# Kernel optimization log

Measured on AMD Instinct MI355X. Metric: run time of the kernel, lower is better.

## Reference

```python
import jax, jax.numpy as jnp
import numpy as np

USER_SIZE = 100000
ITEM_SIZE = 50000
LATENT = 256
BATCH = 8192
ALPHA = 0.8
TAU = 3.0
SHRINK_NORM = 1.0


def setup_inputs() -> dict:
    key = jax.random.key(0)
    k1, k2, k3, k4 = jax.random.split(key, 4)
    # xavier-uniform style init like the torch code
    bu = np.sqrt(6.0 / (USER_SIZE + LATENT)).astype(np.float32)
    bi = np.sqrt(6.0 / (ITEM_SIZE + LATENT)).astype(np.float32)
    user_embed = jax.random.uniform(k1, (USER_SIZE, LATENT), jnp.float32, -bu, bu)
    item_embed = jax.random.uniform(k2, (ITEM_SIZE, LATENT), jnp.float32, -bi, bi)
    u = jax.random.randint(k3, (BATCH,), 0, USER_SIZE)
    p = jax.random.randint(k4, (BATCH,), 0, ITEM_SIZE)
    return {"user_embed": user_embed, "item_embed": item_embed, "u": u, "p": p}


def _spec_smooth(x):
    # x: [B, d] row-normalized embeddings
    # x - alpha * softmax(x x^T * tau, axis=1) @ x, then shrink-norm rescale
    attn = jax.nn.softmax(jnp.einsum('bd,cd->bc', x, x) * TAU, axis=1)  # [B, B]
    y = x - ALPHA * (attn @ x)
    # shrink_norm != 0 branch (static config)
    norm = jnp.linalg.norm(y, axis=1, keepdims=True)
    return y * (norm * SHRINK_NORM)


def reference(user_embed, item_embed, u, p):
    fu = user_embed[u]
    fp = item_embed[p]
    fu = fu / jnp.linalg.norm(fu, axis=1, keepdims=True)
    fp = fp / jnp.linalg.norm(fp, axis=1, keepdims=True)
    fu = _spec_smooth(fu)
    fp = _spec_smooth(fp)
    out = jax.nn.sigmoid(jnp.sum(fu * fp, axis=1))  # [B]
    return -jnp.sum(jnp.log(out)) / BATCH
```

## Files before the change

kernel.cpp:

```cpp
#include <hip/hip_runtime.h>
#include <hip/hip_bf16.h>

#define B_ROWS 8192
#define D_DIM  256
#define QB     64
#define KB     64
#define NT     (B_ROWS / KB)
#define NT2    (NT / 2)
#define ALPHA  0.8f
#define TAU_LOG2E 4.328085122666890f

typedef __attribute__((ext_vector_type(8))) short bf16x8;
typedef __attribute__((ext_vector_type(4))) float f32x4;
typedef __attribute__((ext_vector_type(4))) unsigned short ushort4v;

__device__ inline unsigned short f2bf(float f) {
    unsigned int u = __builtin_bit_cast(unsigned int, f);
    u += 0x7FFF + ((u >> 16) & 1);
    return (unsigned short)(u >> 16);
}

__device__ inline void gl_lds16(const void* g, void* l) {
    __builtin_amdgcn_global_load_lds(
        (const __attribute__((address_space(1))) unsigned int*)g,
        (__attribute__((address_space(3))) unsigned int*)l, 16, 0, 0);
}

__device__ inline void barrier_lgkm() {
    asm volatile("s_waitcnt lgkmcnt(0)" ::: "memory");
    __builtin_amdgcn_s_barrier();
    asm volatile("" ::: "memory");
}
__device__ inline void barrier_all() {
    asm volatile("s_waitcnt vmcnt(0) lgkmcnt(0)" ::: "memory");
    __builtin_amdgcn_s_barrier();
    asm volatile("" ::: "memory");
}

__global__ __launch_bounds__(256) void k_gather_norm(
    const float* __restrict__ ue, const float* __restrict__ ie,
    const int* __restrict__ u, const int* __restrict__ p,
    float* __restrict__ Xf, unsigned short* __restrict__ Xh,
    float* __restrict__ out)
{
    const int b = blockIdx.x * 4 + (threadIdx.x >> 6);
    const int lane = threadIdx.x & 63;
    if (b == 0 && lane == 0) out[0] = 0.0f;
    const int m = b >> 13;
    const int r = b & 8191;
    const float* src = (m == 0) ? (ue + (size_t)u[r] * D_DIM)
                                : (ie + (size_t)p[r] * D_DIM);
    float4 v = ((const float4*)src)[lane];
    float ss = v.x*v.x + v.y*v.y + v.z*v.z + v.w*v.w;
    #pragma unroll
    for (int mask = 32; mask; mask >>= 1) ss += __shfl_xor(ss, mask);
    const float inv = 1.0f / sqrtf(ss);
    v.x *= inv; v.y *= inv; v.z *= inv; v.w *= inv;
    const size_t off = (size_t)(m * B_ROWS + r) * D_DIM + lane * 4;
    *(float4*)(Xf + off) = v;
    ushort4v h = { f2bf(v.x), f2bf(v.y), f2bf(v.z), f2bf(v.w) };
    *(ushort4v*)(Xh + off) = h;
}

__global__ __launch_bounds__(256) void k_transpose(
    const unsigned short* __restrict__ Xh, unsigned short* __restrict__ Xht)
{
    __shared__ unsigned short tile[64 * 84];
    const int bid = blockIdx.x;
    const int m = bid >> 9;
    const int t = bid & 511;
    const int rt = t >> 2, ct = t & 3;
    const int r0 = rt * 64, c0 = ct * 64;
    const int tid = threadIdx.x;
    const unsigned short* src = Xh + (size_t)m * B_ROWS * D_DIM;
    unsigned short* dst = Xht + (size_t)m * D_DIM * B_ROWS;
    #pragma unroll
    for (int ph = 0; ph < 2; ++ph) {
        const int row = ph * 32 + (tid >> 3);
        const int ch = tid & 7;
        const unsigned short* s = src + (size_t)(r0 + row) * D_DIM + c0 + ch * 8;
        ushort4v a = *(const ushort4v*)s;
        ushort4v b = *(const ushort4v*)(s + 4);
        *(ushort4v*)(&tile[row * 84 + ch * 8]) = a;
        *(ushort4v*)(&tile[row * 84 + ch * 8 + 4]) = b;
    }
    __syncthreads();
    #pragma unroll
    for (int ph = 0; ph < 2; ++ph) {
        const int d = ph * 32 + (tid >> 3);
        const int kc = tid & 7;
        ushort4v lo = { tile[(kc*8+0)*84 + d], tile[(kc*8+1)*84 + d],
                        tile[(kc*8+2)*84 + d], tile[(kc*8+3)*84 + d] };
        ushort4v hi = { tile[(kc*8+4)*84 + d], tile[(kc*8+5)*84 + d],
                        tile[(kc*8+6)*84 + d], tile[(kc*8+7)*84 + d] };
        unsigned short* o = dst + (size_t)(c0 + d) * B_ROWS + r0 + kc * 8;
        *(ushort4v*)o = lo;
        *(ushort4v*)(o + 4) = hi;
    }
}

__global__ __launch_bounds__(512, 2) void k_flash_part(
    const unsigned short* __restrict__ Xh,
    const unsigned short* __restrict__ Xht,
    float* __restrict__ Opart,
    float* __restrict__ lsum_part)
{
    __shared__ unsigned char Kls[64 * 512];
    __shared__ unsigned char Vtls[256 * 128];
    __shared__ unsigned char Pls[64 * 128];
    __shared__ float lsum_sh[4][QB];

    const int tid = threadIdx.x;
    const int lane = tid & 63;
    const int w = tid >> 6;
    const int wm = w >> 2;
    const int wn = w & 3;
    const int m  = blockIdx.x >> 8;
    const int qb = (blockIdx.x >> 1) & 127;
    const int h  = blockIdx.x & 1;
    const int q0 = qb * QB;
    const int kvbase = h * (B_ROWS / 2);

    const unsigned short* Xm  = Xh  + (size_t)m * B_ROWS * D_DIM;
    const unsigned short* Xtm = Xht + (size_t)m * D_DIM * B_ROWS;

    bf16x8 qf[2][8];
    #pragma unroll
    for (int mi = 0; mi < 2; ++mi) {
        const unsigned short* qbp = Xm + (size_t)(q0 + wm*32 + mi*16 + (lane & 15)) * D_DIM
                                       + (lane >> 4) * 8;
        #pragma unroll
        for (int kk = 0; kk < 8; ++kk)
            qf[mi][kk] = *(const bf16x8*)(qbp + kk * 32);
    }

    const int kchunk0 = w * 4;
    const int krow_l  = (lane >> 5);
    const int kcol16  = lane & 31;
    const int vd_l    = (lane >> 3);
    const int vkc16   = lane & 7;

    #pragma unroll
    for (int it = 0; it < 4; ++it) {
        const int chunk = kchunk0 + it;
        const int krow = chunk * 2 + krow_l;
        const int kdch = kcol16 ^ (krow & 7);
        gl_lds16(Xm + (size_t)(kvbase + krow) * D_DIM + kdch * 8, &Kls[chunk * 1024]);
        const int vd = chunk * 8 + vd_l;
        const int vkc = vkc16 ^ (vd & 7);
        gl_lds16(Xtm + (size_t)vd * B_ROWS + kvbase + vkc * 8, &Vtls[chunk * 1024]);
    }

    f32x4 o[2][4];
    #pragma unroll
    for (int mi = 0; mi < 2; ++mi)
        #pragma unroll
        for (int nf = 0; nf < 4; ++nf) o[mi][nf] = (f32x4){0.f, 0.f, 0.f, 0.f};
    float lsum[2][4] = {{0.f,0.f,0.f,0.f},{0.f,0.f,0.f,0.f}};

    for (int kt = 0; kt < NT2; ++kt) {
        barrier_all();

        f32x4 s0 = {0.f,0.f,0.f,0.f}, s1 = {0.f,0.f,0.f,0.f};
        {
            const int brow = wn * 16 + (lane & 15);
            const unsigned char* kbase = &Kls[brow * 512];
            const int bswz = (brow & 7) << 4;
            __builtin_amdgcn_s_setprio(1);
            #pragma unroll
            for (int kk = 0; kk < 8; ++kk) {
                const int kb = kk * 64 + ((lane >> 4) * 16);
                bf16x8 bK = *(const bf16x8*)(kbase + (kb ^ bswz));
                s0 = __builtin_amdgcn_mfma_f32_16x16x32_bf16(qf[0][kk], bK, s0, 0, 0, 0);
                s1 = __builtin_amdgcn_mfma_f32_16x16x32_bf16(qf[1][kk], bK, s1, 0, 0, 0);
            }
            __builtin_amdgcn_s_setprio(0);
        }
        #pragma unroll
        for (int i = 0; i < 4; ++i) {
            const float p0 = exp2f(s0[i] * TAU_LOG2E);
            const float p1 = exp2f(s1[i] * TAU_LOG2E);
            lsum[0][i] += p0;
            lsum[1][i] += p1;
            const int pr0 = wm*32 + (lane >> 4) * 4 + i;
            const int pr1 = pr0 + 16;
            const int pc2 = (wn*16 + (lane & 15)) * 2;
            *(unsigned short*)(Pls + pr0*128 + (pc2 ^ ((pr0 & 7) << 4))) = f2bf(p0);
            *(unsigned short*)(Pls + pr1*128 + (pc2 ^ ((pr1 & 7) << 4))) = f2bf(p1);
        }
        barrier_lgkm();

        bf16x8 aP[2][2];
        #pragma unroll
        for (int mi = 0; mi < 2; ++mi)
            #pragma unroll
            for (int ks = 0; ks < 2; ++ks) {
                const int ar = wm*32 + mi*16 + (lane & 15);
                const int akb = ks*64 + ((lane >> 4) * 16);
                aP[mi][ks] = *(const bf16x8*)(Pls + ar*128 + (akb ^ ((ar & 7) << 4)));
            }
        __builtin_amdgcn_s_setprio(1);
        #pragma unroll
        for (int ks = 0; ks < 2; ++ks) {
            #pragma unroll
            for (int nf = 0; nf < 4; ++nf) {
                const int dr = wn*64 + nf*16 + (lane & 15);
                const int kb2 = ks*64 + ((lane >> 4) * 16);
                bf16x8 bV = *(const bf16x8*)(&Vtls[dr*128 + (kb2 ^ ((dr & 7) << 4))]);
                o[0][nf] = __builtin_amdgcn_mfma_f32_16x16x32_bf16(aP[0][ks], bV, o[0][nf], 0, 0, 0);
                o[1][nf] = __builtin_amdgcn_mfma_f32_16x16x32_bf16(aP[1][ks], bV, o[1][nf], 0, 0, 0);
            }
        }
        __builtin_amdgcn_s_setprio(0);
        barrier_lgkm();

        if (kt + 1 < NT2) {
            const int kvn = kvbase + (kt + 1) * KB;
            #pragma unroll
            for (int it = 0; it < 4; ++it) {
                const int chunk = kchunk0 + it;
                const int krow = chunk * 2 + krow_l;
                const int kdch = kcol16 ^ (krow & 7);
                gl_lds16(Xm + (size_t)(kvn + krow) * D_DIM + kdch * 8, &Kls[chunk * 1024]);
                const int vd = chunk * 8 + vd_l;
                const int vkc = vkc16 ^ (vd & 7);
                gl_lds16(Xtm + (size_t)vd * B_ROWS + kvn + vkc * 8, &Vtls[chunk * 1024]);
            }
        }
    }

    #pragma unroll
    for (int mi = 0; mi < 2; ++mi)
        #pragma unroll
        for (int i = 0; i < 4; ++i) {
            float v = lsum[mi][i];
            v += __shfl_xor(v, 1); v += __shfl_xor(v, 2);
            v += __shfl_xor(v, 4); v += __shfl_xor(v, 8);
            if ((lane & 15) == 0)
                lsum_sh[wn][wm*32 + mi*16 + (lane >> 4)*4 + i] = v;
        }
    __syncthreads();
    if (tid < QB)
        lsum_part[(size_t)blockIdx.x * QB + tid] =
            lsum_sh[0][tid] + lsum_sh[1][tid] + lsum_sh[2][tid] + lsum_sh[3][tid];

    float* Ob = Opart + (size_t)blockIdx.x * QB * D_DIM;
    #pragma unroll
    for (int mi = 0; mi < 2; ++mi)
        #pragma unroll
        for (int nf = 0; nf < 4; ++nf)
            #pragma unroll
            for (int i = 0; i < 4; ++i) {
                const int row = wm*32 + mi*16 + (lane >> 4)*4 + i;
                const int col = wn*64 + nf*16 + (lane & 15);
                Ob[row * D_DIM + col] = o[mi][nf][i];
            }
}

__global__ __launch_bounds__(256) void k_combine_loss(
    const float* __restrict__ Xf, const float* __restrict__ Opart,
    const float* __restrict__ lsum_part, float* __restrict__ out)
{
    __shared__ float part[4];
    const int w = threadIdx.x >> 6;
    const int lane = threadIdx.x & 63;
    const int r = blockIdx.x * 4 + w;
    const int qb = r >> 6, ri = r & 63;

    float y[2][4];
    float nrm[2];
    #pragma unroll
    for (int m = 0; m < 2; ++m) {
        const int blk0 = m * 256 + qb * 2;
        const float l = lsum_part[(size_t)blk0 * QB + ri]
                      + lsum_part[(size_t)(blk0 + 1) * QB + ri];
        const float c = ALPHA / l;
        const float4 x  = *(const float4*)(Xf + ((size_t)m * B_ROWS + r) * D_DIM + lane * 4);
        const float4 o0 = *(const float4*)(Opart + ((size_t)blk0 * QB + ri) * D_DIM + lane * 4);
        const float4 o1 = *(const float4*)(Opart + ((size_t)(blk0 + 1) * QB + ri) * D_DIM + lane * 4);
        y[m][0] = x.x - c * (o0.x + o1.x);
        y[m][1] = x.y - c * (o0.y + o1.y);
        y[m][2] = x.z - c * (o0.z + o1.z);
        y[m][3] = x.w - c * (o0.w + o1.w);
        float s = y[m][0]*y[m][0] + y[m][1]*y[m][1] + y[m][2]*y[m][2] + y[m][3]*y[m][3];
        #pragma unroll
        for (int mask = 32; mask; mask >>= 1) s += __shfl_xor(s, mask);
        nrm[m] = s;
    }
    float d = y[0][0]*y[1][0] + y[0][1]*y[1][1] + y[0][2]*y[1][2] + y[0][3]*y[1][3];
    #pragma unroll
    for (int mask = 32; mask; mask >>= 1) d += __shfl_xor(d, mask);
    if (lane == 0) {
        const float z = sqrtf(nrm[0] * nrm[1]) * d;
        part[w] = log1pf(expf(-z));
    }
    __syncthreads();
    if (threadIdx.x == 0)
        atomicAdd(out, (part[0] + part[1] + part[2] + part[3]) * (1.0f / 8192.0f));
}

__global__ __launch_bounds__(512, 2) void k_flash(
    const unsigned short* __restrict__ Xh, const unsigned short* __restrict__ Xht,
    float* __restrict__ Xf)
{
    __shared__ unsigned char Kls[2][64 * 512];
    __shared__ unsigned char Vtls[2][256 * 128];
    __shared__ unsigned char Pls[64 * 128];
    __shared__ float lsum_sh[4][QB];
    __shared__ float nrm_sh[4][QB];

    const int tid = threadIdx.x;
    const int lane = tid & 63;
    const int w = tid >> 6;
    const int wm = w >> 2;
    const int wn = w & 3;
    const int m = blockIdx.x >> 7;
    const int q0 = (blockIdx.x & 127) * QB;

    const unsigned short* Xm  = Xh  + (size_t)m * B_ROWS * D_DIM;
    const unsigned short* Xtm = Xht + (size_t)m * D_DIM * B_ROWS;
    float* Xfm = Xf + (size_t)m * B_ROWS * D_DIM;

    bf16x8 qf[2][8];
    #pragma unroll
    for (int mi = 0; mi < 2; ++mi) {
        const unsigned short* qbp = Xm + (size_t)(q0 + wm*32 + mi*16 + (lane & 15)) * D_DIM
                                       + (lane >> 4) * 8;
        #pragma unroll
        for (int kk = 0; kk < 8; ++kk)
            qf[mi][kk] = *(const bf16x8*)(qbp + kk * 32);
    }

    const int kchunk0 = w * 4;
    const int krow_l  = (lane >> 5);
    const int kcol16  = lane & 31;
    const int vd_l    = (lane >> 3);
    const int vkc16   = lane & 7;

    #pragma unroll
    for (int it = 0; it < 4; ++it) {
        const int chunk = kchunk0 + it;
        const int krow = chunk * 2 + krow_l;
        const int kdch = kcol16 ^ (krow & 7);
        gl_lds16(Xm + (size_t)krow * D_DIM + kdch * 8, &Kls[0][chunk * 1024]);
        const int vd = chunk * 8 + vd_l;
        const int vkc = vkc16 ^ (vd & 7);
        gl_lds16(Xtm + (size_t)vd * B_ROWS + vkc * 8, &Vtls[0][chunk * 1024]);
    }
    barrier_all();

    f32x4 o[2][4];
    #pragma unroll
    for (int mi = 0; mi < 2; ++mi)
        #pragma unroll
        for (int nf = 0; nf < 4; ++nf) o[mi][nf] = (f32x4){0.f, 0.f, 0.f, 0.f};
    float lsum[2][4] = {{0.f,0.f,0.f,0.f},{0.f,0.f,0.f,0.f}};
    int cur = 0;

    for (int kt = 0; kt < NT; ++kt) {
        const int nxt = cur ^ 1;
        if (kt + 1 < NT) {
            const int kvn = (kt + 1) * KB;
            #pragma unroll
            for (int it = 0; it < 4; ++it) {
                const int chunk = kchunk0 + it;
                const int krow = chunk * 2 + krow_l;
                const int kdch = kcol16 ^ (krow & 7);
                gl_lds16(Xm + (size_t)(kvn + krow) * D_DIM + kdch * 8, &Kls[nxt][chunk * 1024]);
                const int vd = chunk * 8 + vd_l;
                const int vkc = vkc16 ^ (vd & 7);
                gl_lds16(Xtm + (size_t)vd * B_ROWS + kvn + vkc * 8, &Vtls[nxt][chunk * 1024]);
            }
        }
        f32x4 s0 = {0.f,0.f,0.f,0.f}, s1 = {0.f,0.f,0.f,0.f};
        {
            const int brow = wn * 16 + (lane & 15);
            const unsigned char* kbase = &Kls[cur][brow * 512];
            const int bswz = (brow & 7) << 4;
            #pragma unroll
            for (int kk = 0; kk < 8; ++kk) {
                const int kb = kk * 64 + ((lane >> 4) * 16);
                bf16x8 bK = *(const bf16x8*)(kbase + (kb ^ bswz));
                s0 = __builtin_amdgcn_mfma_f32_16x16x32_bf16(qf[0][kk], bK, s0, 0, 0, 0);
                s1 = __builtin_amdgcn_mfma_f32_16x16x32_bf16(qf[1][kk], bK, s1, 0, 0, 0);
            }
        }
        #pragma unroll
        for (int i = 0; i < 4; ++i) {
            const float p0 = exp2f(s0[i] * TAU_LOG2E);
            const float p1 = exp2f(s1[i] * TAU_LOG2E);
            lsum[0][i] += p0;
            lsum[1][i] += p1;
            const int pr0 = wm*32 + (lane >> 4) * 4 + i;
            const int pr1 = pr0 + 16;
            const int pc2 = (wn*16 + (lane & 15)) * 2;
            *(unsigned short*)(Pls + pr0*128 + (pc2 ^ ((pr0 & 7) << 4))) = f2bf(p0);
            *(unsigned short*)(Pls + pr1*128 + (pc2 ^ ((pr1 & 7) << 4))) = f2bf(p1);
        }
        barrier_lgkm();
        bf16x8 aP[2][2];
        #pragma unroll
        for (int mi = 0; mi < 2; ++mi)
            #pragma unroll
            for (int ks = 0; ks < 2; ++ks) {
                const int ar = wm*32 + mi*16 + (lane & 15);
                const int akb = ks*64 + ((lane >> 4) * 16);
                aP[mi][ks] = *(const bf16x8*)(Pls + ar*128 + (akb ^ ((ar & 7) << 4)));
            }
        #pragma unroll
        for (int ks = 0; ks < 2; ++ks) {
            #pragma unroll
            for (int nf = 0; nf < 4; ++nf) {
                const int dr = wn*64 + nf*16 + (lane & 15);
                const int kb2 = ks*64 + ((lane >> 4) * 16);
                bf16x8 bV = *(const bf16x8*)(&Vtls[cur][dr*128 + (kb2 ^ ((dr & 7) << 4))]);
                o[0][nf] = __builtin_amdgcn_mfma_f32_16x16x32_bf16(aP[0][ks], bV, o[0][nf], 0, 0, 0);
                o[1][nf] = __builtin_amdgcn_mfma_f32_16x16x32_bf16(aP[1][ks], bV, o[1][nf], 0, 0, 0);
            }
        }
        barrier_all();
        cur = nxt;
    }

    #pragma unroll
    for (int mi = 0; mi < 2; ++mi)
        #pragma unroll
        for (int i = 0; i < 4; ++i) {
            float v = lsum[mi][i];
            v += __shfl_xor(v, 1); v += __shfl_xor(v, 2);
            v += __shfl_xor(v, 4); v += __shfl_xor(v, 8);
            if ((lane & 15) == 0)
                lsum_sh[wn][wm*32 + mi*16 + (lane >> 4)*4 + i] = v;
        }
    __syncthreads();

    float nrm[2][4] = {{0.f,0.f,0.f,0.f},{0.f,0.f,0.f,0.f}};
    #pragma unroll
    for (int mi = 0; mi < 2; ++mi)
        #pragma unroll
        for (int nf = 0; nf < 4; ++nf)
            #pragma unroll
            for (int i = 0; i < 4; ++i) {
                const int row = wm*32 + mi*16 + (lane >> 4)*4 + i;
                const int col = wn*64 + nf*16 + (lane & 15);
                const float x = Xfm[(size_t)(q0 + row) * D_DIM + col];
                const float lt = lsum_sh[0][row] + lsum_sh[1][row]
                               + lsum_sh[2][row] + lsum_sh[3][row];
                const float yv = x - (ALPHA / lt) * o[mi][nf][i];
                o[mi][nf][i] = yv;
                nrm[mi][i] += yv * yv;
            }
    #pragma unroll
    for (int mi = 0; mi < 2; ++mi)
        #pragma unroll
        for (int i = 0; i < 4; ++i) {
            float v = nrm[mi][i];
            v += __shfl_xor(v, 1); v += __shfl_xor(v, 2);
            v += __shfl_xor(v, 4); v += __shfl_xor(v, 8);
            if ((lane & 15) == 0)
                nrm_sh[wn][wm*32 + mi*16 + (lane >> 4)*4 + i] = v;
        }
    __syncthreads();
    #pragma unroll
    for (int mi = 0; mi < 2; ++mi)
        #pragma unroll
        for (int nf = 0; nf < 4; ++nf)
            #pragma unroll
            for (int i = 0; i < 4; ++i) {
                const int row = wm*32 + mi*16 + (lane >> 4)*4 + i;
                const int col = wn*64 + nf*16 + (lane & 15);
                const float scale = sqrtf(nrm_sh[0][row] + nrm_sh[1][row]
                                        + nrm_sh[2][row] + nrm_sh[3][row]);
                Xfm[(size_t)(q0 + row) * D_DIM + col] = o[mi][nf][i] * scale;
            }
}

__global__ __launch_bounds__(256) void k_loss(
    const float* __restrict__ Yu, const float* __restrict__ Yp,
    float* __restrict__ out)
{
    __shared__ float part[4];
    const int w = threadIdx.x >> 6;
    const int lane = threadIdx.x & 63;
    float acc = 0.0f;
    #pragma unroll
    for (int r = 0; r < 8; ++r) {
        const int row = blockIdx.x * 32 + w * 8 + r;
        const float4 a = *(const float4*)(Yu + (size_t)row * D_DIM + lane * 4);
        const float4 b = *(const float4*)(Yp + (size_t)row * D_DIM + lane * 4);
        float dot = a.x*b.x + a.y*b.y + a.z*b.z + a.w*b.w;
        #pragma unroll
        for (int mask = 32; mask; mask >>= 1) dot += __shfl_xor(dot, mask);
        if (lane == 0) acc += log1pf(expf(-dot));
    }
    if (lane == 0) part[w] = acc;
    __syncthreads();
    if (threadIdx.x == 0) {
        const float s = part[0] + part[1] + part[2] + part[3];
        atomicAdd(out, s * (1.0f / 8192.0f));
    }
}

extern "C" void kernel_launch(void* const* d_in, const int* in_sizes, int n_in,
                              void* d_out, int out_size, void* d_ws, size_t ws_size,
                              hipStream_t stream) {
    const float* ue = (const float*)d_in[0];
    const float* ie = (const float*)d_in[1];
    const int*   u  = (const int*)d_in[2];
    const int*   p  = (const int*)d_in[3];
    float* out = (float*)d_out;

    char* ws = (char*)d_ws;
    float* Xf            = (float*)ws;
    unsigned short* Xh   = (unsigned short*)(ws + (16u << 20));
    unsigned short* Xht  = (unsigned short*)(ws + (24u << 20));
    float* Opart         = (float*)(ws + (32u << 20));
    float* lsum_part     = (float*)(ws + (64u << 20));

    const size_t need = (64u << 20) + (128u << 10);

    k_gather_norm<<<4096, 256, 0, stream>>>(ue, ie, u, p, Xf, Xh, out);
    k_transpose <<<1024, 256, 0, stream>>>(Xh, Xht);
    if (ws_size >= need) {
        k_flash_part  <<<512, 512, 0, stream>>>(Xh, Xht, Opart, lsum_part);
        k_combine_loss<<<2048, 256, 0, stream>>>(Xf, Opart, lsum_part, out);
    } else {
        k_flash<<<256, 512, 0, stream>>>(Xh, Xht, Xf);
        k_loss <<<256, 256, 0, stream>>>(Xf, Xf + (size_t)B_ROWS * D_DIM, out);
    }
}
```

Baseline: 454.2 us.

## Double query tile to 128 rows and double-buffer K/V in split flash kernel

Each block of the split-KV flash kernel now processes 128 query rows instead of 64, with each wave holding four 16-row query fragments. This halves the grid and doubles reuse of each K/V tile loaded into LDS. K and V tiles are now double-buffered so the next tile's global-to-LDS load overlaps the current tile's MFMA work. The cost is more LDS and registers per block, and with only 256 blocks on a large-CU device, occupancy and load balance may suffer. The combine kernel's indexing is updated to match the new partial layout, and the setprio hints are dropped.

New measurement: 417.8 us. 1.09x faster.

```diff
diff --git a/kernel.cpp b/kernel.cpp
--- a/kernel.cpp
+++ b/kernel.cpp
@@ -3,10 +3,7 @@
 
 #define B_ROWS 8192
 #define D_DIM  256
-#define QB     64
 #define KB     64
-#define NT     (B_ROWS / KB)
-#define NT2    (NT / 2)
 #define ALPHA  0.8f
 #define TAU_LOG2E 4.328085122666890f
 
@@ -105,29 +102,29 @@
     float* __restrict__ Opart,
     float* __restrict__ lsum_part)
 {
-    __shared__ unsigned char Kls[64 * 512];
-    __shared__ unsigned char Vtls[256 * 128];
-    __shared__ unsigned char Pls[64 * 128];
-    __shared__ float lsum_sh[4][QB];
+    __shared__ unsigned char Kls[2][64 * 512];
+    __shared__ unsigned char Vtls[2][256 * 128];
+    __shared__ unsigned char Pls[128 * 128];
+    __shared__ float lsum_sh[4][128];
 
     const int tid = threadIdx.x;
     const int lane = tid & 63;
     const int w = tid >> 6;
     const int wm = w >> 2;
     const int wn = w & 3;
-    const int m  = blockIdx.x >> 8;
-    const int qb = (blockIdx.x >> 1) & 127;
+    const int m  = blockIdx.x >> 7;
+    const int qb = (blockIdx.x >> 1) & 63;
     const int h  = blockIdx.x & 1;
-    const int q0 = qb * QB;
+    const int q0 = qb * 128;
     const int kvbase = h * (B_ROWS / 2);
 
     const unsigned short* Xm  = Xh  + (size_t)m * B_ROWS * D_DIM;
     const unsigned short* Xtm = Xht + (size_t)m * D_DIM * B_ROWS;
 
-    bf16x8 qf[2][8];
-    #pragma unroll
-    for (int mi = 0; mi < 2; ++mi) {
-        const unsigned short* qbp = Xm + (size_t)(q0 + wm*32 + mi*16 + (lane & 15)) * D_DIM
+    bf16x8 qf[4][8];
+    #pragma unroll
+    for (int mi = 0; mi < 4; ++mi) {
+        const unsigned short* qbp = Xm + (size_t)(q0 + wm*64 + mi*16 + (lane & 15)) * D_DIM
                                        + (lane >> 4) * 8;
         #pragma unroll
         for (int kk = 0; kk < 8; ++kk)
@@ -140,16 +137,221 @@
     const int vd_l    = (lane >> 3);
     const int vkc16   = lane & 7;
 
+    const int brow  = wn * 16 + (lane & 15);
+    const int bswz  = (brow & 7) << 4;
+    const int kqoff = (lane >> 4) * 16;
+
     #pragma unroll
     for (int it = 0; it < 4; ++it) {
         const int chunk = kchunk0 + it;
         const int krow = chunk * 2 + krow_l;
         const int kdch = kcol16 ^ (krow & 7);
-        gl_lds16(Xm + (size_t)(kvbase + krow) * D_DIM + kdch * 8, &Kls[chunk * 1024]);
+        gl_lds16(Xm + (size_t)(kvbase + krow) * D_DIM + kdch * 8, &Kls[0][chunk * 1024]);
         const int vd = chunk * 8 + vd_l;
         const int vkc = vkc16 ^ (vd & 7);
-        gl_lds16(Xtm + (size_t)vd * B_ROWS + kvbase + vkc * 8, &Vtls[chunk * 1024]);
-    }
+        gl_lds16(Xtm + (size_t)vd * B_ROWS + kvbase + vkc * 8, &Vtls[0][chunk * 1024]);
+    }
+    barrier_all();
+
+    f32x4 o[4][4];
+    #pragma unroll
+    for (int mi = 0; mi < 4; ++mi)
+        #pragma unroll
+        for (int nf = 0; nf < 4; ++nf) o[mi][nf] = (f32x4){0.f, 0.f, 0.f, 0.f};
+    float lsum[4][4] = {{0.f,0.f,0.f,0.f},{0.f,0.f,0.f,0.f},
+                        {0.f,0.f,0.f,0.f},{0.f,0.f,0.f,0.f}};
+    int cur = 0;
+
+    for (int kt = 0; kt < 64; ++kt) {
+        const int nxt = cur ^ 1;
+        if (kt + 1 < 64) {
+            const int kvn = kvbase + (kt + 1) * KB;
+            #pragma unroll
+            for (int it = 0; it < 4; ++it) {
+                const int chunk = kchunk0 + it;
+                const int krow = chunk * 2 + krow_l;
+                const int kdch = kcol16 ^ (krow & 7);
+                gl_lds16(Xm + (size_t)(kvn + krow) * D_DIM + kdch * 8,
+                         &Kls[nxt][chunk * 1024]);
+                const int vd = chunk * 8 + vd_l;
+                const int vkc = vkc16 ^ (vd & 7);
+                gl_lds16(Xtm + (size_t)vd * B_ROWS + kvn + vkc * 8,
+                         &Vtls[nxt][chunk * 1024]);
+            }
+        }
+
+        f32x4 s0 = {0.f,0.f,0.f,0.f}, s1 = {0.f,0.f,0.f,0.f};
+        f32x4 s2 = {0.f,0.f,0.f,0.f}, s3 = {0.f,0.f,0.f,0.f};
+        {
+            const unsigned char* kbase = &Kls[cur][brow * 512];
+            #pragma unroll
+            for (int kk = 0; kk < 8; ++kk) {
+                bf16x8 bK = *(const bf16x8*)(kbase + ((kk * 64 + kqoff) ^ bswz));
+                s0 = __builtin_amdgcn_mfma_f32_16x16x32_bf16(qf[0][kk], bK, s0, 0, 0, 0);
+                s1 = __builtin_amdgcn_mfma_f32_16x16x32_bf16(qf[1][kk], bK, s1, 0, 0, 0);
+                s2 = __builtin_amdgcn_mfma_f32_16x16x32_bf16(qf[2][kk], bK, s2, 0, 0, 0);
+                s3 = __builtin_amdgcn_mfma_f32_16x16x32_bf16(qf[3][kk], bK, s3, 0, 0, 0);
+            }
+        }
+        #pragma unroll
+        for (int i = 0; i < 4; ++i) {
+            const float p0 = exp2f(s0[i] * TAU_LOG2E);
+            const float p1 = exp2f(s1[i] * TAU_LOG2E);
+            const float p2 = exp2f(s2[i] * TAU_LOG2E);
+            const float p3 = exp2f(s3[i] * TAU_LOG2E);
+            lsum[0][i] += p0;  lsum[1][i] += p1;
+            lsum[2][i] += p2;  lsum[3][i] += p3;
+            const int prb = wm*64 + (lane >> 4) * 4 + i;
+            const int pc2 = (wn*16 + (lane & 15)) * 2;
+            *(unsigned short*)(Pls + (prb   )*128 + (pc2 ^ (((prb   ) & 7) << 4))) = f2bf(p0);
+            *(unsigned short*)(Pls + (prb+16)*128 + (pc2 ^ (((prb+16) & 7) << 4))) = f2bf(p1);
+            *(unsigned short*)(Pls + (prb+32)*128 + (pc2 ^ (((prb+32) & 7) << 4))) = f2bf(p2);
+            *(unsigned short*)(Pls + (prb+48)*128 + (pc2 ^ (((prb+48) & 7) << 4))) = f2bf(p3);
+        }
+        barrier_lgkm();
+
+        #pragma unroll
+        for (int ks = 0; ks < 2; ++ks) {
+            bf16x8 aP[4];
+            #pragma unroll
+            for (int mi = 0; mi < 4; ++mi) {
+                const int ar = wm*64 + mi*16 + (lane & 15);
+                aP[mi] = *(const bf16x8*)(Pls + ar*128 + ((ks*64 + kqoff) ^ ((ar & 7) << 4)));
+            }
+            #pragma unroll
+            for (int nf = 0; nf < 4; ++nf) {
+                const int dr = wn*64 + nf*16 + (lane & 15);
+                bf16x8 bV = *(const bf16x8*)(&Vtls[cur][dr*128 + ((ks*64 + kqoff) ^ ((dr & 7) << 4))]);
+                o[0][nf] = __builtin_amdgcn_mfma_f32_16x16x32_bf16(aP[0], bV, o[0][nf], 0, 0, 0);
+                o[1][nf] = __builtin_amdgcn_mfma_f32_16x16x32_bf16(aP[1], bV, o[1][nf], 0, 0, 0);
+                o[2][nf] = __builtin_amdgcn_mfma_f32_16x16x32_bf16(aP[2], bV, o[2][nf], 0, 0, 0);
+                o[3][nf] = __builtin_amdgcn_mfma_f32_16x16x32_bf16(aP[3], bV, o[3][nf], 0, 0, 0);
+            }
+        }
+
+        barrier_all();
+        cur = nxt;
+    }
+
+    #pragma unroll
+    for (int mi = 0; mi < 4; ++mi)
+        #pragma unroll
+        for (int i = 0; i < 4; ++i) {
+            float v = lsum[mi][i];
+            v += __shfl_xor(v, 1); v += __shfl_xor(v, 2);
+            v += __shfl_xor(v, 4); v += __shfl_xor(v, 8);
+            if ((lane & 15) == 0)
+                lsum_sh[wn][wm*64 + mi*16 + (lane >> 4)*4 + i] = v;
+        }
+    __syncthreads();
+    if (tid < 128)
+        lsum_part[(size_t)blockIdx.x * 128 + tid] =
+            lsum_sh[0][tid] + lsum_sh[1][tid] + lsum_sh[2][tid] + lsum_sh[3][tid];
+
+    float* Ob = Opart + (size_t)blockIdx.x * 128 * D_DIM;
+    #pragma unroll
+    for (int mi = 0; mi < 4; ++mi)
+        #pragma unroll
+        for (int nf = 0; nf < 4; ++nf)
+            #pragma unroll
+            for (int i = 0; i < 4; ++i) {
+                const int row = wm*64 + mi*16 + (lane >> 4)*4 + i;
+                const int col = wn*64 + nf*16 + (lane & 15);
+                Ob[row * D_DIM + col] = o[mi][nf][i];
+            }
+}
+
+__global__ __launch_bounds__(256) void k_combine_loss(
+    const float* __restrict__ Xf, const float* __restrict__ Opart,
+    const float* __restrict__ lsum_part, float* __restrict__ out)
+{
+    __shared__ float part[4];
+    const int w = threadIdx.x >> 6;
+    const int lane = threadIdx.x & 63;
+    const int r = blockIdx.x * 4 + w;
+    const int qb = r >> 7, ri = r & 127;
+
+    float y[2][4];
+    float nrm[2];
+    #pragma unroll
+    for (int m = 0; m < 2; ++m) {
+        const int blk0 = m * 128 + qb * 2;
+        const float l = lsum_part[(size_t)blk0 * 128 + ri]
+                      + lsum_part[(size_t)(blk0 + 1) * 128 + ri];
+        const float c = ALPHA / l;
+        const float4 x  = *(const float4*)(Xf + ((size_t)m * B_ROWS + r) * D_DIM + lane * 4);
+        const float4 o0 = *(const float4*)(Opart + ((size_t)blk0 * 128 + ri) * D_DIM + lane * 4);
+        const float4 o1 = *(const float4*)(Opart + ((size_t)(blk0 + 1) * 128 + ri) * D_DIM + lane * 4);
+        y[m][0] = x.x - c * (o0.x + o1.x);
+        y[m][1] = x.y - c * (o0.y + o1.y);
+        y[m][2] = x.z - c * (o0.z + o1.z);
+        y[m][3] = x.w - c * (o0.w + o1.w);
+        float s = y[m][0]*y[m][0] + y[m][1]*y[m][1] + y[m][2]*y[m][2] + y[m][3]*y[m][3];
+        #pragma unroll
+        for (int mask = 32; mask; mask >>= 1) s += __shfl_xor(s, mask);
+        nrm[m] = s;
+    }
+    float d = y[0][0]*y[1][0] + y[0][1]*y[1][1] + y[0][2]*y[1][2] + y[0][3]*y[1][3];
+    #pragma unroll
+    for (int mask = 32; mask; mask >>= 1) d += __shfl_xor(d, mask);
+    if (lane == 0) {
+        const float z = sqrtf(nrm[0] * nrm[1]) * d;
+        part[w] = log1pf(expf(-z));
+    }
+    __syncthreads();
+    if (threadIdx.x == 0)
+        atomicAdd(out, (part[0] + part[1] + part[2] + part[3]) * (1.0f / 8192.0f));
+}
+
+__global__ __launch_bounds__(512, 2) void k_flash(
+    const unsigned short* __restrict__ Xh, const unsigned short* __restrict__ Xht,
+    float* __restrict__ Xf)
+{
+    __shared__ unsigned char Kls[2][64 * 512];
+    __shared__ unsigned char Vtls[2][256 * 128];
+    __shared__ unsigned char Pls[64 * 128];
+    __shared__ float lsum_sh[4][64];
+    __shared__ float nrm_sh[4][64];
+
+    const int tid = threadIdx.x;
+    const int lane = tid & 63;
+    const int w = tid >> 6;
+    const int wm = w >> 2;
+    const int wn = w & 3;
+    const int m = blockIdx.x >> 7;
+    const int q0 = (blockIdx.x & 127) * 64;
+
+    const unsigned short* Xm  = Xh  + (size_t)m * B_ROWS * D_DIM;
+    const unsigned short* Xtm = Xht + (size_t)m * D_DIM * B_ROWS;
+    float* Xfm = Xf + (size_t)m * B_ROWS * D_DIM;
+
+    bf16x8 qf[2][8];
+    #pragma unroll
+    for (int mi = 0; mi < 2; ++mi) {
+        const unsigned short* qbp = Xm + (size_t)(q0 + wm*32 + mi*16 + (lane & 15)) * D_DIM
+                                       + (lane >> 4) * 8;
+        #pragma unroll
+        for (int kk = 0; kk < 8; ++kk)
+            qf[mi][kk] = *(const bf16x8*)(qbp + kk * 32);
+    }
+
+    const int kchunk0 = w * 4;
+    const int krow_l  = (lane >> 5);
+    const int kcol16  = lane & 31;
+    const int vd_l    = (lane >> 3);
+    const int vkc16   = lane & 7;
+
+    #pragma unroll
+    for (int it = 0; it < 4; ++it) {
+        const int chunk = kchunk0 + it;
+        const int krow = chunk * 2 + krow_l;
+        const int kdch = kcol16 ^ (krow & 7);
+        gl_lds16(Xm + (size_t)krow * D_DIM + kdch * 8, &Kls[0][chunk * 1024]);
+        const int vd = chunk * 8 + vd_l;
+        const int vkc = vkc16 ^ (vd & 7);
+        gl_lds16(Xtm + (size_t)vd * B_ROWS + vkc * 8, &Vtls[0][chunk * 1024]);
+    }
+    barrier_all();
 
     f32x4 o[2][4];
     #pragma unroll
@@ -157,16 +359,28 @@
         #pragma unroll
         for (int nf = 0; nf < 4; ++nf) o[mi][nf] = (f32x4){0.f, 0.f, 0.f, 0.f};
     float lsum[2][4] = {{0.f,0.f,0.f,0.f},{0.f,0.f,0.f,0.f}};
-
-    for (int kt = 0; kt < NT2; ++kt) {
-        barrier_all();
-
+    int cur = 0;
+
+    for (int kt = 0; kt < 128; ++kt) {
+        const int nxt = cur ^ 1;
+        if (kt + 1 < 128) {
+            const int kvn = (kt + 1) * KB;
+            #pragma unroll
+            for (int it = 0; it < 4; ++it) {
+                const int chunk = kchunk0 + it;
+                const int krow = chunk * 2 + krow_l;
+                const int kdch = kcol16 ^ (krow & 7);
+                gl_lds16(Xm + (size_t)(kvn + krow) * D_DIM + kdch * 8, &Kls[nxt][chunk * 1024]);
+                const int vd = chunk * 8 + vd_l;
+                const int vkc = vkc16 ^ (vd & 7);
+                gl_lds16(Xtm + (size_t)vd * B_ROWS + kvn + vkc * 8, &Vtls[nxt][chunk * 1024]);
+            }
+        }
         f32x4 s0 = {0.f,0.f,0.f,0.f}, s1 = {0.f,0.f,0.f,0.f};
         {
             const int brow = wn * 16 + (lane & 15);
-            const unsigned char* kbase = &Kls[brow * 512];
+            const unsigned char* kbase = &Kls[cur][brow * 512];
             const int bswz = (brow & 7) << 4;
-            __builtin_amdgcn_s_setprio(1);
             #pragma unroll
             for (int kk = 0; kk < 8; ++kk) {
                 const int kb = kk * 64 + ((lane >> 4) * 16);
@@ -174,7 +388,6 @@
                 s0 = __builtin_amdgcn_mfma_f32_16x16x32_bf16(qf[0][kk], bK, s0, 0, 0, 0);
                 s1 = __builtin_amdgcn_mfma_f32_16x16x32_bf16(qf[1][kk], bK, s1, 0, 0, 0);
             }
-            __builtin_amdgcn_s_setprio(0);
         }
         #pragma unroll
         for (int i = 0; i < 4; ++i) {
@@ -189,215 +402,6 @@
             *(unsigned short*)(Pls + pr1*128 + (pc2 ^ ((pr1 & 7) << 4))) = f2bf(p1);
         }
         barrier_lgkm();
-
-        bf16x8 aP[2][2];
-        #pragma unroll
-        for (int mi = 0; mi < 2; ++mi)
-            #pragma unroll
-            for (int ks = 0; ks < 2; ++ks) {
-                const int ar = wm*32 + mi*16 + (lane & 15);
-                const int akb = ks*64 + ((lane >> 4) * 16);
-                aP[mi][ks] = *(const bf16x8*)(Pls + ar*128 + (akb ^ ((ar & 7) << 4)));
-            }
-        __builtin_amdgcn_s_setprio(1);
-        #pragma unroll
-        for (int ks = 0; ks < 2; ++ks) {
-            #pragma unroll
-            for (int nf = 0; nf < 4; ++nf) {
-                const int dr = wn*64 + nf*16 + (lane & 15);
-                const int kb2 = ks*64 + ((lane >> 4) * 16);
-                bf16x8 bV = *(const bf16x8*)(&Vtls[dr*128 + (kb2 ^ ((dr & 7) << 4))]);
-                o[0][nf] = __builtin_amdgcn_mfma_f32_16x16x32_bf16(aP[0][ks], bV, o[0][nf], 0, 0, 0);
-                o[1][nf] = __builtin_amdgcn_mfma_f32_16x16x32_bf16(aP[1][ks], bV, o[1][nf], 0, 0, 0);
-            }
-        }
-        __builtin_amdgcn_s_setprio(0);
-        barrier_lgkm();
-
-        if (kt + 1 < NT2) {
-            const int kvn = kvbase + (kt + 1) * KB;
-            #pragma unroll
-            for (int it = 0; it < 4; ++it) {
-                const int chunk = kchunk0 + it;
-                const int krow = chunk * 2 + krow_l;
-                const int kdch = kcol16 ^ (krow & 7);
-                gl_lds16(Xm + (size_t)(kvn + krow) * D_DIM + kdch * 8, &Kls[chunk * 1024]);
-                const int vd = chunk * 8 + vd_l;
-                const int vkc = vkc16 ^ (vd & 7);
-                gl_lds16(Xtm + (size_t)vd * B_ROWS + kvn + vkc * 8, &Vtls[chunk * 1024]);
-            }
-        }
-    }
-
-    #pragma unroll
-    for (int mi = 0; mi < 2; ++mi)
-        #pragma unroll
-        for (int i = 0; i < 4; ++i) {
-            float v = lsum[mi][i];
-            v += __shfl_xor(v, 1); v += __shfl_xor(v, 2);
-            v += __shfl_xor(v, 4); v += __shfl_xor(v, 8);
-            if ((lane & 15) == 0)
-                lsum_sh[wn][wm*32 + mi*16 + (lane >> 4)*4 + i] = v;
-        }
-    __syncthreads();
-    if (tid < QB)
-        lsum_part[(size_t)blockIdx.x * QB + tid] =
-            lsum_sh[0][tid] + lsum_sh[1][tid] + lsum_sh[2][tid] + lsum_sh[3][tid];
-
-    float* Ob = Opart + (size_t)blockIdx.x * QB * D_DIM;
-    #pragma unroll
-    for (int mi = 0; mi < 2; ++mi)
-        #pragma unroll
-        for (int nf = 0; nf < 4; ++nf)
-            #pragma unroll
-            for (int i = 0; i < 4; ++i) {
-                const int row = wm*32 + mi*16 + (lane >> 4)*4 + i;
-                const int col = wn*64 + nf*16 + (lane & 15);
-                Ob[row * D_DIM + col] = o[mi][nf][i];
-            }
-}
-
-__global__ __launch_bounds__(256) void k_combine_loss(
-    const float* __restrict__ Xf, const float* __restrict__ Opart,
-    const float* __restrict__ lsum_part, float* __restrict__ out)
-{
-    __shared__ float part[4];
-    const int w = threadIdx.x >> 6;
-    const int lane = threadIdx.x & 63;
-    const int r = blockIdx.x * 4 + w;
-    const int qb = r >> 6, ri = r & 63;
-
-    float y[2][4];
-    float nrm[2];
-    #pragma unroll
-    for (int m = 0; m < 2; ++m) {
-        const int blk0 = m * 256 + qb * 2;
-        const float l = lsum_part[(size_t)blk0 * QB + ri]
-                      + lsum_part[(size_t)(blk0 + 1) * QB + ri];
-        const float c = ALPHA / l;
-        const float4 x  = *(const float4*)(Xf + ((size_t)m * B_ROWS + r) * D_DIM + lane * 4);
-        const float4 o0 = *(const float4*)(Opart + ((size_t)blk0 * QB + ri) * D_DIM + lane * 4);
-        const float4 o1 = *(const float4*)(Opart + ((size_t)(blk0 + 1) * QB + ri) * D_DIM + lane * 4);
-        y[m][0] = x.x - c * (o0.x + o1.x);
-        y[m][1] = x.y - c * (o0.y + o1.y);
-        y[m][2] = x.z - c * (o0.z + o1.z);
-        y[m][3] = x.w - c * (o0.w + o1.w);
-        float s = y[m][0]*y[m][0] + y[m][1]*y[m][1] + y[m][2]*y[m][2] + y[m][3]*y[m][3];
-        #pragma unroll
-        for (int mask = 32; mask; mask >>= 1) s += __shfl_xor(s, mask);
-        nrm[m] = s;
-    }
-    float d = y[0][0]*y[1][0] + y[0][1]*y[1][1] + y[0][2]*y[1][2] + y[0][3]*y[1][3];
-    #pragma unroll
-    for (int mask = 32; mask; mask >>= 1) d += __shfl_xor(d, mask);
-    if (lane == 0) {
-        const float z = sqrtf(nrm[0] * nrm[1]) * d;
-        part[w] = log1pf(expf(-z));
-    }
-    __syncthreads();
-    if (threadIdx.x == 0)
-        atomicAdd(out, (part[0] + part[1] + part[2] + part[3]) * (1.0f / 8192.0f));
-}
-
-__global__ __launch_bounds__(512, 2) void k_flash(
-    const unsigned short* __restrict__ Xh, const unsigned short* __restrict__ Xht,
-    float* __restrict__ Xf)
-{
-    __shared__ unsigned char Kls[2][64 * 512];
-    __shared__ unsigned char Vtls[2][256 * 128];
-    __shared__ unsigned char Pls[64 * 128];
-    __shared__ float lsum_sh[4][QB];
-    __shared__ float nrm_sh[4][QB];
-
-    const int tid = threadIdx.x;
-    const int lane = tid & 63;
-    const int w = tid >> 6;
-    const int wm = w >> 2;
-    const int wn = w & 3;
-    const int m = blockIdx.x >> 7;
-    const int q0 = (blockIdx.x & 127) * QB;
-
-    const unsigned short* Xm  = Xh  + (size_t)m * B_ROWS * D_DIM;
-    const unsigned short* Xtm = Xht + (size_t)m * D_DIM * B_ROWS;
-    float* Xfm = Xf + (size_t)m * B_ROWS * D_DIM;
-
-    bf16x8 qf[2][8];
-    #pragma unroll
-    for (int mi = 0; mi < 2; ++mi) {
-        const unsigned short* qbp = Xm + (size_t)(q0 + wm*32 + mi*16 + (lane & 15)) * D_DIM
-                                       + (lane >> 4) * 8;
-        #pragma unroll
-        for (int kk = 0; kk < 8; ++kk)
-            qf[mi][kk] = *(const bf16x8*)(qbp + kk * 32);
-    }
-
-    const int kchunk0 = w * 4;
-    const int krow_l  = (lane >> 5);
-    const int kcol16  = lane & 31;
-    const int vd_l    = (lane >> 3);
-    const int vkc16   = lane & 7;
-
-    #pragma unroll
-    for (int it = 0; it < 4; ++it) {
-        const int chunk = kchunk0 + it;
-        const int krow = chunk * 2 + krow_l;
-        const int kdch = kcol16 ^ (krow & 7);
-        gl_lds16(Xm + (size_t)krow * D_DIM + kdch * 8, &Kls[0][chunk * 1024]);
-        const int vd = chunk * 8 + vd_l;
-        const int vkc = vkc16 ^ (vd & 7);
-        gl_lds16(Xtm + (size_t)vd * B_ROWS + vkc * 8, &Vtls[0][chunk * 1024]);
-    }
-    barrier_all();
-
-    f32x4 o[2][4];
-    #pragma unroll
-    for (int mi = 0; mi < 2; ++mi)
-        #pragma unroll
-        for (int nf = 0; nf < 4; ++nf) o[mi][nf] = (f32x4){0.f, 0.f, 0.f, 0.f};
-    float lsum[2][4] = {{0.f,0.f,0.f,0.f},{0.f,0.f,0.f,0.f}};
-    int cur = 0;
-
-    for (int kt = 0; kt < NT; ++kt) {
-        const int nxt = cur ^ 1;
-        if (kt + 1 < NT) {
-            const int kvn = (kt + 1) * KB;
-            #pragma unroll
-            for (int it = 0; it < 4; ++it) {
-                const int chunk = kchunk0 + it;
-                const int krow = chunk * 2 + krow_l;
-                const int kdch = kcol16 ^ (krow & 7);
-                gl_lds16(Xm + (size_t)(kvn + krow) * D_DIM + kdch * 8, &Kls[nxt][chunk * 1024]);
-                const int vd = chunk * 8 + vd_l;
-                const int vkc = vkc16 ^ (vd & 7);
-                gl_lds16(Xtm + (size_t)vd * B_ROWS + kvn + vkc * 8, &Vtls[nxt][chunk * 1024]);
-            }
-        }
-        f32x4 s0 = {0.f,0.f,0.f,0.f}, s1 = {0.f,0.f,0.f,0.f};
-        {
-            const int brow = wn * 16 + (lane & 15);
-            const unsigned char* kbase = &Kls[cur][brow * 512];
-            const int bswz = (brow & 7) << 4;
-            #pragma unroll
-            for (int kk = 0; kk < 8; ++kk) {
-                const int kb = kk * 64 + ((lane >> 4) * 16);
-                bf16x8 bK = *(const bf16x8*)(kbase + (kb ^ bswz));
-                s0 = __builtin_amdgcn_mfma_f32_16x16x32_bf16(qf[0][kk], bK, s0, 0, 0, 0);
-                s1 = __builtin_amdgcn_mfma_f32_16x16x32_bf16(qf[1][kk], bK, s1, 0, 0, 0);
-            }
-        }
-        #pragma unroll
-        for (int i = 0; i < 4; ++i) {
-            const float p0 = exp2f(s0[i] * TAU_LOG2E);
-            const float p1 = exp2f(s1[i] * TAU_LOG2E);
-            lsum[0][i] += p0;
-            lsum[1][i] += p1;
-            const int pr0 = wm*32 + (lane >> 4) * 4 + i;
-            const int pr1 = pr0 + 16;
-            const int pc2 = (wn*16 + (lane & 15)) * 2;
-            *(unsigned short*)(Pls + pr0*128 + (pc2 ^ ((pr0 & 7) << 4))) = f2bf(p0);
-            *(unsigned short*)(Pls + pr1*128 + (pc2 ^ ((pr1 & 7) << 4))) = f2bf(p1);
-        }
-        barrier_lgkm();
         bf16x8 aP[2][2];
         #pragma unroll
         for (int mi = 0; mi < 2; ++mi)
@@ -522,7 +526,7 @@
     k_gather_norm<<<4096, 256, 0, stream>>>(ue, ie, u, p, Xf, Xh, out);
     k_transpose <<<1024, 256, 0, stream>>>(Xh, Xht);
     if (ws_size >= need) {
-        k_flash_part  <<<512, 512, 0, stream>>>(Xh, Xht, Opart, lsum_part);
+        k_flash_part  <<<256, 512, 0, stream>>>(Xh, Xht, Opart, lsum_part);
         k_combine_loss<<<2048, 256, 0, stream>>>(Xf, Opart, lsum_part, out);
     } else {
         k_flash<<<256, 512, 0, stream>>>(Xh, Xht, Xf);
```

## Stream V from global directly and remap blocks to share KV across XCDs

Applied to the files above, without the earlier changes.

The split-KV flash kernel stops staging the transposed V tile in LDS and reads V fragments straight from global memory into registers for the PV MFMAs. This frees LDS so occupancy can rise to 4 blocks per CU. The block index is remapped so neighbouring blocks share the matrix and KV half, and the partial outputs are written with nontemporal stores. It also drops the s_setprio hints and moves the next K prefetch ahead of the PV compute. The cost is uncoalesced, higher-latency global V reads on the critical path and more VGPR pressure under the tighter launch bounds.

Result: slower. 818.1 us (+80.1%).

```diff
diff --git a/kernel.cpp b/kernel.cpp
--- a/kernel.cpp
+++ b/kernel.cpp
@@ -3,10 +3,7 @@
 
 #define B_ROWS 8192
 #define D_DIM  256
-#define QB     64
 #define KB     64
-#define NT     (B_ROWS / KB)
-#define NT2    (NT / 2)
 #define ALPHA  0.8f
 #define TAU_LOG2E 4.328085122666890f
 
@@ -99,26 +96,27 @@
     }
 }
 
-__global__ __launch_bounds__(512, 2) void k_flash_part(
+__global__ __launch_bounds__(512, 4) void k_flash_part(
     const unsigned short* __restrict__ Xh,
     const unsigned short* __restrict__ Xht,
     float* __restrict__ Opart,
     float* __restrict__ lsum_part)
 {
     __shared__ unsigned char Kls[64 * 512];
-    __shared__ unsigned char Vtls[256 * 128];
     __shared__ unsigned char Pls[64 * 128];
-    __shared__ float lsum_sh[4][QB];
+    __shared__ float lsum_sh[4][64];
 
     const int tid = threadIdx.x;
     const int lane = tid & 63;
     const int w = tid >> 6;
     const int wm = w >> 2;
     const int wn = w & 3;
-    const int m  = blockIdx.x >> 8;
-    const int qb = (blockIdx.x >> 1) & 127;
-    const int h  = blockIdx.x & 1;
-    const int q0 = qb * QB;
+    const int c  = blockIdx.x & 7;
+    const int m  = (c >> 2) & 1;
+    const int h  = (c >> 1) & 1;
+    const int qb = ((blockIdx.x >> 3) << 1) | (c & 1);
+    const int lblk = m * 256 + qb * 2 + h;
+    const int q0 = qb * 64;
     const int kvbase = h * (B_ROWS / 2);
 
     const unsigned short* Xm  = Xh  + (size_t)m * B_ROWS * D_DIM;
@@ -137,8 +135,10 @@
     const int kchunk0 = w * 4;
     const int krow_l  = (lane >> 5);
     const int kcol16  = lane & 31;
-    const int vd_l    = (lane >> 3);
-    const int vkc16   = lane & 7;
+
+    const int brow  = wn * 16 + (lane & 15);
+    const int bswz  = (brow & 7) << 4;
+    const int kqoff = (lane >> 4) * 16;
 
     #pragma unroll
     for (int it = 0; it < 4; ++it) {
@@ -146,10 +146,8 @@
         const int krow = chunk * 2 + krow_l;
         const int kdch = kcol16 ^ (krow & 7);
         gl_lds16(Xm + (size_t)(kvbase + krow) * D_DIM + kdch * 8, &Kls[chunk * 1024]);
-        const int vd = chunk * 8 + vd_l;
-        const int vkc = vkc16 ^ (vd & 7);
-        gl_lds16(Xtm + (size_t)vd * B_ROWS + kvbase + vkc * 8, &Vtls[chunk * 1024]);
-    }
+    }
+    barrier_all();
 
     f32x4 o[2][4];
     #pragma unroll
@@ -158,23 +156,18 @@
         for (int nf = 0; nf < 4; ++nf) o[mi][nf] = (f32x4){0.f, 0.f, 0.f, 0.f};
     float lsum[2][4] = {{0.f,0.f,0.f,0.f},{0.f,0.f,0.f,0.f}};
 
-    for (int kt = 0; kt < NT2; ++kt) {
-        barrier_all();
+    for (int kt = 0; kt < 64; ++kt) {
+        const int kv0 = kvbase + kt * KB;
 
         f32x4 s0 = {0.f,0.f,0.f,0.f}, s1 = {0.f,0.f,0.f,0.f};
         {
-            const int brow = wn * 16 + (lane & 15);
             const unsigned char* kbase = &Kls[brow * 512];
-            const int bswz = (brow & 7) << 4;
-            __builtin_amdgcn_s_setprio(1);
             #pragma unroll
             for (int kk = 0; kk < 8; ++kk) {
-                const int kb = kk * 64 + ((lane >> 4) * 16);
-                bf16x8 bK = *(const bf16x8*)(kbase + (kb ^ bswz));
+                bf16x8 bK = *(const bf16x8*)(kbase + ((kk * 64 + kqoff) ^ bswz));
                 s0 = __builtin_amdgcn_mfma_f32_16x16x32_bf16(qf[0][kk], bK, s0, 0, 0, 0);
                 s1 = __builtin_amdgcn_mfma_f32_16x16x32_bf16(qf[1][kk], bK, s1, 0, 0, 0);
             }
-            __builtin_amdgcn_s_setprio(0);
         }
         #pragma unroll
         for (int i = 0; i < 4; ++i) {
@@ -190,43 +183,37 @@
         }
         barrier_lgkm();
 
-        bf16x8 aP[2][2];
-        #pragma unroll
-        for (int mi = 0; mi < 2; ++mi)
-            #pragma unroll
-            for (int ks = 0; ks < 2; ++ks) {
-                const int ar = wm*32 + mi*16 + (lane & 15);
-                const int akb = ks*64 + ((lane >> 4) * 16);
-                aP[mi][ks] = *(const bf16x8*)(Pls + ar*128 + (akb ^ ((ar & 7) << 4)));
-            }
-        __builtin_amdgcn_s_setprio(1);
-        #pragma unroll
-        for (int ks = 0; ks < 2; ++ks) {
-            #pragma unroll
-            for (int nf = 0; nf < 4; ++nf) {
-                const int dr = wn*64 + nf*16 + (lane & 15);
-                const int kb2 = ks*64 + ((lane >> 4) * 16);
-                bf16x8 bV = *(const bf16x8*)(&Vtls[dr*128 + (kb2 ^ ((dr & 7) << 4))]);
-                o[0][nf] = __builtin_amdgcn_mfma_f32_16x16x32_bf16(aP[0][ks], bV, o[0][nf], 0, 0, 0);
-                o[1][nf] = __builtin_amdgcn_mfma_f32_16x16x32_bf16(aP[1][ks], bV, o[1][nf], 0, 0, 0);
-            }
-        }
-        __builtin_amdgcn_s_setprio(0);
-        barrier_lgkm();
-
-        if (kt + 1 < NT2) {
+        if (kt + 1 < 64) {
             const int kvn = kvbase + (kt + 1) * KB;
             #pragma unroll
             for (int it = 0; it < 4; ++it) {
                 const int chunk = kchunk0 + it;
                 const int krow = chunk * 2 + krow_l;
                 const int kdch = kcol16 ^ (krow & 7);
-                gl_lds16(Xm + (size_t)(kvn + krow) * D_DIM + kdch * 8, &Kls[chunk * 1024]);
-                const int vd = chunk * 8 + vd_l;
-                const int vkc = vkc16 ^ (vd & 7);
-                gl_lds16(Xtm + (size_t)vd * B_ROWS + kvn + vkc * 8, &Vtls[chunk * 1024]);
-            }
-        }
+                gl_lds16(Xm + (size_t)(kvn + krow) * D_DIM + kdch * 8,
+                         &Kls[chunk * 1024]);
+            }
+        }
+
+        #pragma unroll
+        for (int ks = 0; ks < 2; ++ks) {
+            bf16x8 aP[2];
+            #pragma unroll
+            for (int mi = 0; mi < 2; ++mi) {
+                const int ar = wm*32 + mi*16 + (lane & 15);
+                aP[mi] = *(const bf16x8*)(Pls + ar*128 + ((ks*64 + kqoff) ^ ((ar & 7) << 4)));
+            }
+            #pragma unroll
+            for (int nf = 0; nf < 4; ++nf) {
+                const int dr = wn*64 + nf*16 + (lane & 15);
+                bf16x8 bV = *(const bf16x8*)(Xtm + (size_t)dr * B_ROWS + kv0
+                                             + ks*32 + (lane >> 4) * 8);
+                o[0][nf] = __builtin_amdgcn_mfma_f32_16x16x32_bf16(aP[0], bV, o[0][nf], 0, 0, 0);
+                o[1][nf] = __builtin_amdgcn_mfma_f32_16x16x32_bf16(aP[1], bV, o[1][nf], 0, 0, 0);
+            }
+        }
+
+        barrier_all();
     }
 
     #pragma unroll
@@ -240,11 +227,12 @@
                 lsum_sh[wn][wm*32 + mi*16 + (lane >> 4)*4 + i] = v;
         }
     __syncthreads();
-    if (tid < QB)
-        lsum_part[(size_t)blockIdx.x * QB + tid] =
-            lsum_sh[0][tid] + lsum_sh[1][tid] + lsum_sh[2][tid] + lsum_sh[3][tid];
-
-    float* Ob = Opart + (size_t)blockIdx.x * QB * D_DIM;
+    if (tid < 64)
+        __builtin_nontemporal_store(
+            lsum_sh[0][tid] + lsum_sh[1][tid] + lsum_sh[2][tid] + lsum_sh[3][tid],
+            &lsum_part[(size_t)lblk * 64 + tid]);
+
+    float* Ob = Opart + (size_t)lblk * 64 * D_DIM;
     #pragma unroll
     for (int mi = 0; mi < 2; ++mi)
         #pragma unroll
@@ -253,7 +241,7 @@
             for (int i = 0; i < 4; ++i) {
                 const int row = wm*32 + mi*16 + (lane >> 4)*4 + i;
                 const int col = wn*64 + nf*16 + (lane & 15);
-                Ob[row * D_DIM + col] = o[mi][nf][i];
+                __builtin_nontemporal_store(o[mi][nf][i], &Ob[row * D_DIM + col]);
             }
 }
 
@@ -272,12 +260,12 @@
     #pragma unroll
     for (int m = 0; m < 2; ++m) {
         const int blk0 = m * 256 + qb * 2;
-        const float l = lsum_part[(size_t)blk0 * QB + ri]
-                      + lsum_part[(size_t)(blk0 + 1) * QB + ri];
+        const float l = lsum_part[(size_t)blk0 * 64 + ri]
+                      + lsum_part[(size_t)(blk0 + 1) * 64 + ri];
         const float c = ALPHA / l;
         const float4 x  = *(const float4*)(Xf + ((size_t)m * B_ROWS + r) * D_DIM + lane * 4);
-        const float4 o0 = *(const float4*)(Opart + ((size_t)blk0 * QB + ri) * D_DIM + lane * 4);
-        const float4 o1 = *(const float4*)(Opart + ((size_t)(blk0 + 1) * QB + ri) * D_DIM + lane * 4);
+        const float4 o0 = *(const float4*)(Opart + ((size_t)blk0 * 64 + ri) * D_DIM + lane * 4);
+        const float4 o1 = *(const float4*)(Opart + ((size_t)(blk0 + 1) * 64 + ri) * D_DIM + lane * 4);
         y[m][0] = x.x - c * (o0.x + o1.x);
         y[m][1] = x.y - c * (o0.y + o1.y);
         y[m][2] = x.z - c * (o0.z + o1.z);
@@ -306,8 +294,8 @@
     __shared__ unsigned char Kls[2][64 * 512];
     __shared__ unsigned char Vtls[2][256 * 128];
     __shared__ unsigned char Pls[64 * 128];
-    __shared__ float lsum_sh[4][QB];
-    __shared__ float nrm_sh[4][QB];
+    __shared__ float lsum_sh[4][64];
+    __shared__ float nrm_sh[4][64];
 
     const int tid = threadIdx.x;
     const int lane = tid & 63;
@@ -315,7 +303,7 @@
     const int wm = w >> 2;
     const int wn = w & 3;
     const int m = blockIdx.x >> 7;
-    const int q0 = (blockIdx.x & 127) * QB;
+    const int q0 = (blockIdx.x & 127) * 64;
 
     const unsigned short* Xm  = Xh  + (size_t)m * B_ROWS * D_DIM;
     const unsigned short* Xtm = Xht + (size_t)m * D_DIM * B_ROWS;
@@ -357,9 +345,9 @@
     float lsum[2][4] = {{0.f,0.f,0.f,0.f},{0.f,0.f,0.f,0.f}};
     int cur = 0;
 
-    for (int kt = 0; kt < NT; ++kt) {
+    for (int kt = 0; kt < 128; ++kt) {
         const int nxt = cur ^ 1;
-        if (kt + 1 < NT) {
+        if (kt + 1 < 128) {
             const int kvn = (kt + 1) * KB;
             #pragma unroll
             for (int it = 0; it < 4; ++it) {
```
